# Kernel optimization log

Measured on AMD Instinct MI355X. Metric: run time of the kernel, lower is better.

## Reference

```python
import jax, jax.numpy as jnp
import numpy as np

B, N, K = 2, 8192, 16
C_IN, C_OUT, HID = 64, 256, 256
L, HEADS, DKQV = 2, 8, 32
D = HEADS * DKQV  # 256


def setup_inputs() -> dict:
    key = jax.random.key(0)
    ks = jax.random.split(key, 20)
    s = 0.02
    inp = {
        "xyzs": jax.random.normal(ks[0], (B, N, 3), jnp.float32),
        "features": jax.random.normal(ks[1], (B, N, C_IN), jnp.float32),
        "k_graph": jax.random.randint(ks[2], (B, N, K), 0, N),
        "W_in": jax.random.normal(ks[3], (C_IN, HID), jnp.float32) * s,
        "b_in": jnp.zeros((HID,), jnp.float32),
        "Wq": jax.random.normal(ks[4], (L, HID, D), jnp.float32) * s,
        "bq": jnp.zeros((L, D), jnp.float32),
        "Wk": jax.random.normal(ks[5], (L, HID, D), jnp.float32) * s,
        "bk": jnp.zeros((L, D), jnp.float32),
        "Wv": jax.random.normal(ks[6], (L, HID, D), jnp.float32) * s,
        "bv": jnp.zeros((L, D), jnp.float32),
        "Wp": jax.random.normal(ks[7], (L, 3, D), jnp.float32) * s,
        "bp": jnp.zeros((L, D), jnp.float32),
        "Wo": jax.random.normal(ks[8], (L, D, HID), jnp.float32) * s,
        "bo": jnp.zeros((L, HID), jnp.float32),
        "W_out": jax.random.normal(ks[9], (HID, C_OUT), jnp.float32) * s,
        "b_out": jnp.zeros((C_OUT,), jnp.float32),
    }
    return inp


def _gather(f, idx):
    # f: [B,N,D], idx: [B,N,K] -> [B,N,K,D]
    return jnp.take_along_axis(f[:, None], idx[..., None], axis=2)


def _knn_attn(xyz, f, idx, Wq, bq, Wk, bk, Wv, bv, Wp, bp, Wo, bo):
    b, n, _ = f.shape
    q = f @ Wq + bq                      # [B,N,D]
    k = f @ Wk + bk
    v = f @ Wv + bv
    k_nb = _gather(k, idx)               # [B,N,K,D]
    v_nb = _gather(v, idx)
    rel = xyz[:, :, None, :] - _gather(xyz, idx)   # [B,N,K,3]
    pos = rel @ Wp + bp                  # [B,N,K,D] relative positional encoding
    kh = (k_nb + pos).reshape(b, n, K, HEADS, DKQV)
    vh = (v_nb + pos).reshape(b, n, K, HEADS, DKQV)
    qh = q.reshape(b, n, HEADS, DKQV)
    logits = jnp.einsum('bnhd,bnkhd->bnhk', qh, kh) / np.sqrt(DKQV)
    attn = jax.nn.softmax(logits, axis=-1)          # softmax over K neighbors
    o = jnp.einsum('bnhk,bnkhd->bnhd', attn, vh).reshape(b, n, D)
    return o @ Wo + bo


def reference(xyzs, features, k_graph, W_in, b_in, Wq, bq, Wk, bk, Wv, bv,
              Wp, bp, Wo, bo, W_out, b_out):
    f = features @ W_in + b_in
    for l in range(L):
        res = f  # res_connection=True
        f = _knn_attn(xyzs, f, k_graph, Wq[l], bq[l], Wk[l], bk[l],
                      Wv[l], bv[l], Wp[l], bp[l], Wo[l], bo[l]) + res
    out = f @ W_out + b_out
    return jax.nn.leaky_relu(out, negative_slope=0.01)
```

## Files before the change

### kernel.cpp

```cpp
#include <hip/hip_runtime.h>
#include <hip/hip_bf16.h>

typedef __attribute__((ext_vector_type(8))) short bf16x8;
typedef __attribute__((ext_vector_type(4))) float f32x4;
typedef __attribute__((ext_vector_type(2))) _Float16 h2;
typedef __attribute__((ext_vector_type(8))) _Float16 h8;
typedef unsigned int uint;

constexpr int NPTS = 8192;
constexpr int BPTS = 16384;
constexpr int KNN  = 16;

__device__ __forceinline__ void gload16(const void* g, void* l) {
    __builtin_amdgcn_global_load_lds(
        (const __attribute__((address_space(1))) unsigned int*)g,
        (__attribute__((address_space(3))) unsigned int*)l, 16, 0, 0);
}

__device__ __forceinline__ uint packbf2(float a, float b) {
    union { __hip_bfloat16 h; unsigned short u; } ua, ub;
    ua.h = __float2bfloat16(a); ub.h = __float2bfloat16(b);
    return (uint)ua.u | ((uint)ub.u << 16);
}

template<int KD, bool RES, int OUTT, bool LRELU>
__global__ __launch_bounds__(256) void gemm_mfma(
    const __hip_bfloat16* __restrict__ A,
    const __hip_bfloat16* __restrict__ Bt,
    const float* __restrict__ b0, const float* __restrict__ b1,
    const float* __restrict__ b2,
    const __hip_bfloat16* __restrict__ res,
    void* __restrict__ Cout, int M, int N)
{
    __shared__ __align__(16) __hip_bfloat16 As[128 * 64];
    __shared__ __align__(16) __hip_bfloat16 Bs[128 * 64];

    const int tid  = threadIdx.x;
    const int lane = tid & 63;
    const int wid  = tid >> 6;
    const int wm   = (wid >> 1) * 64;
    const int wn   = (wid & 1) * 64;
    const int bm   = blockIdx.y * 128;
    const int bn   = blockIdx.x * 128;

    const int srow8 = lane >> 3;
    const int sslot = (lane & 7) ^ srow8;
    const int r = lane & 15;
    const int g = lane >> 4;

    f32x4 acc[4][4] = {};

    for (int k0 = 0; k0 < KD; k0 += 64) {
        #pragma unroll
        for (int p = 0; p < 4; ++p) {
            const int rowA = p * 32 + wid * 8 + srow8;
            gload16(&A[(size_t)(bm + rowA) * KD + k0 + sslot * 8],
                    (char*)As + (p * 32 + wid * 8) * 128);
            gload16(&Bt[(size_t)(bn + rowA) * KD + k0 + sslot * 8],
                    (char*)Bs + (p * 32 + wid * 8) * 128);
        }
        __syncthreads();

        bf16x8 af[2][4], bfr[2][4];
        #pragma unroll
        for (int s = 0; s < 2; ++s) {
            const int physA = (s * 4 + g) ^ (r & 7);
            #pragma unroll
            for (int mi = 0; mi < 4; ++mi)
                af[s][mi] = *(const bf16x8*)((const char*)As + (wm + mi * 16 + r) * 128 + physA * 16);
            #pragma unroll
            for (int ni = 0; ni < 4; ++ni)
                bfr[s][ni] = *(const bf16x8*)((const char*)Bs + (wn + ni * 16 + r) * 128 + physA * 16);
        }
        #pragma unroll
        for (int s = 0; s < 2; ++s)
            #pragma unroll
            for (int mi = 0; mi < 4; ++mi)
                #pragma unroll
                for (int ni = 0; ni < 4; ++ni)
                    acc[mi][ni] = __builtin_amdgcn_mfma_f32_16x16x32_bf16(
                        af[s][mi], bfr[s][ni], acc[mi][ni], 0, 0, 0);
        __syncthreads();
    }

    #pragma unroll
    for (int ni = 0; ni < 4; ++ni) {
        const int col = bn + wn + ni * 16 + r;
        const float* bsel = (col < 256) ? b0 : (col < 512 ? b1 : b2);
        const float bias = bsel[col & 255];
        #pragma unroll
        for (int mi = 0; mi < 4; ++mi) {
            #pragma unroll
            for (int q = 0; q < 4; ++q) {
                const int row = bm + wm + mi * 16 + g * 4 + q;
                float v = acc[mi][ni][q] + bias;
                if (RES)  v += __bfloat162float(res[(size_t)row * N + col]);
                if (LRELU) v = v > 0.f ? v : 0.01f * v;
                if (OUTT == 0)      ((float*)Cout)[(size_t)row * N + col] = v;
                else if (OUTT == 1) ((__hip_bfloat16*)Cout)[(size_t)row * N + col] = __float2bfloat16(v);
                else                ((_Float16*)Cout)[(size_t)row * N + col] = (_Float16)v;
            }
        }
    }
}

__global__ __launch_bounds__(256) void prep_kernel(
    const float* __restrict__ W_in, const float* __restrict__ Wq,
    const float* __restrict__ Wk,  const float* __restrict__ Wv,
    const float* __restrict__ Wo,  const float* __restrict__ W_out,
    const float* __restrict__ features,
    const float* __restrict__ Wp,  const float* __restrict__ bp,
    __hip_bfloat16* __restrict__ WtIn,  __hip_bfloat16* __restrict__ WtQKV,
    __hip_bfloat16* __restrict__ WtO,   __hip_bfloat16* __restrict__ WtOut,
    __hip_bfloat16* __restrict__ featb, _Float16* __restrict__ Wpb)
{
    const int b = blockIdx.x;
    if (b < 592) {
        const float* srcs[10] = {W_in, Wq, Wk, Wv, Wq + 65536, Wk + 65536,
                                 Wv + 65536, Wo, Wo + 65536, W_out};
        __hip_bfloat16* dsts[10] = {
            WtIn, WtQKV, WtQKV + 65536, WtQKV + 131072,
            WtQKV + 196608, WtQKV + 262144, WtQKV + 327680,
            WtO, WtO + 65536, WtOut};
        const int Ks[10]    = {64,256,256,256,256,256,256,256,256,256};
        const int start[10] = {0,16,80,144,208,272,336,400,464,528};
        int j = 0;
        #pragma unroll
        for (int i = 1; i < 10; ++i) if (b >= start[i]) j = i;
        const int t  = b - start[j];
        const int Kd = Ks[j];
        const int ntk = Kd >> 5;
        const int tn = t / ntk;
        const int tk = t - tn * ntk;

        __shared__ float s[32][33];
        const int tx = threadIdx.x & 31, ty = threadIdx.x >> 5;
        const float* src = srcs[j];
        #pragma unroll
        for (int i = 0; i < 4; ++i)
            s[ty + i * 8][tx] = src[(size_t)(tk * 32 + ty + i * 8) * 256 + tn * 32 + tx];
        __syncthreads();
        __hip_bfloat16* dst = dsts[j];
        #pragma unroll
        for (int i = 0; i < 4; ++i)
            dst[(size_t)(tn * 32 + ty + i * 8) * Kd + tk * 32 + tx] =
                __float2bfloat16(s[tx][ty + i * 8]);
    } else if (b < 1616) {
        const int i = (b - 592) * 1024 + threadIdx.x * 4;
        const float4 v = *(const float4*)&features[i];
        __hip_bfloat16 tmp[4] = {__float2bfloat16(v.x), __float2bfloat16(v.y),
                                 __float2bfloat16(v.z), __float2bfloat16(v.w)};
        *(uint2*)&featb[i] = *(const uint2*)tmp;
    } else {
        const int e8 = threadIdx.x * 8;
        const int l  = e8 >> 10;
        const int rr = (e8 >> 8) & 3;
        const int c  = e8 & 255;
        const float* src = (rr < 3) ? (Wp + (size_t)l * 768 + rr * 256 + c)
                                    : (bp + (size_t)l * 256 + c);
        const float4 f0 = ((const float4*)src)[0];
        const float4 f1 = ((const float4*)src)[1];
        _Float16 t[8] = {(_Float16)f0.x, (_Float16)f0.y, (_Float16)f0.z, (_Float16)f0.w,
                         (_Float16)f1.x, (_Float16)f1.y, (_Float16)f1.z, (_Float16)f1.w};
        *(uint4*)&Wpb[(size_t)l * 1024 + rr * 256 + c] = *(const uint4*)t;
    }
}

__global__ __launch_bounds__(256) void knn_attn_kernel(
    const float* __restrict__ xyz,
    const int*   __restrict__ idx,
    const _Float16* __restrict__ qkv,
    const _Float16* __restrict__ Wpb,
    __hip_bfloat16* __restrict__ o)
{
    const int tid = threadIdx.x;
    const int pt  = tid >> 7;
    const int lt  = tid & 127;
    const int p0  = blockIdx.x * 2;
    const int p   = p0 + pt;
    const int h   = lt >> 4;
    const int k   = lt & 15;

    __shared__ float s_rel[2][KNN][3];
    __shared__ float s_wq[2][8][4];
    __shared__ float s_attn[2][8][KNN];
    __shared__ float s_arel[2][8][3];
    __shared__ __align__(16) _Float16 v_lds[2][KNN][256];

    const int jrow = ((p >> 13) << 13) + idx[p * KNN + k];
    const h8* qp = (const h8*)(qkv + (size_t)p * 768 + h * 32);
    const h8* kp = (const h8*)(qkv + (size_t)jrow * 768 + 256 + h * 32);
    const h8 q0 = qp[0], q1 = qp[1];
    const h8 k0 = kp[0], k1 = kp[1];

    {
        const int w = tid >> 6, ln = tid & 63;
        #pragma unroll
        for (int c = 0; c < 4; ++c) {
            const int grE = w * 8 + c * 2;
            const int gr  = grE + (ln >> 5);
            const int ptw = grE >> 4, kkE = grE & 15;
            const int pg  = p0 + (gr >> 4);
            const int jr  = ((pg >> 13) << 13) + idx[pg * KNN + (gr & 15)];
            gload16(qkv + (size_t)jr * 768 + 512 + (ln & 31) * 8,
                    (char*)&v_lds[ptw][kkE][0]);
        }
    }

    if (tid < 32) {
        const int pp = tid >> 4, kk = tid & 15;
        const int pg = p0 + pp;
        const int jr = ((pg >> 13) << 13) + idx[pg * KNN + kk];
        s_rel[pp][kk][0] = xyz[pg * 3 + 0] - xyz[jr * 3 + 0];
        s_rel[pp][kk][1] = xyz[pg * 3 + 1] - xyz[jr * 3 + 1];
        s_rel[pp][kk][2] = xyz[pg * 3 + 2] - xyz[jr * 3 + 2];
    } else if (tid < 96) {
        const int t2 = tid - 32;
        const int pp = t2 >> 5, hh = (t2 >> 2) & 7, j = t2 & 3;
        const h8* qr = (const h8*)(qkv + (size_t)(p0 + pp) * 768 + hh * 32);
        const h8* wr = (const h8*)(Wpb + j * 256 + hh * 32);
        const h8 a0 = qr[0], a1 = qr[1], b0 = wr[0], b1 = wr[1];
        float acc = 0.f;
        #pragma unroll
        for (int i = 0; i < 4; ++i)
            acc = __builtin_amdgcn_fdot2(((const h2*)&a0)[i], ((const h2*)&b0)[i], acc, false);
        #pragma unroll
        for (int i = 0; i < 4; ++i)
            acc = __builtin_amdgcn_fdot2(((const h2*)&a1)[i], ((const h2*)&b1)[i], acc, false);
        s_wq[pp][hh][j] = acc;
    }

    float dot = 0.f;
    #pragma unroll
    for (int i = 0; i < 4; ++i)
        dot = __builtin_amdgcn_fdot2(((const h2*)&q0)[i], ((const h2*)&k0)[i], dot, false);
    #pragma unroll
    for (int i = 0; i < 4; ++i)
        dot = __builtin_amdgcn_fdot2(((const h2*)&q1)[i], ((const h2*)&k1)[i], dot, false);
    __syncthreads();

    const float r0 = s_rel[pt][k][0], r1 = s_rel[pt][k][1], r2 = s_rel[pt][k][2];
    const float logit = (dot + r0 * s_wq[pt][h][0] + r1 * s_wq[pt][h][1]
                             + r2 * s_wq[pt][h][2] + s_wq[pt][h][3])
                        * 0.1767766952966369f;
    float mx = logit;
    #pragma unroll
    for (int off = 8; off >= 1; off >>= 1)
        mx = fmaxf(mx, __shfl_xor(mx, off, 16));
    const float e = __expf(logit - mx);
    float den = e;
    #pragma unroll
    for (int off = 8; off >= 1; off >>= 1)
        den += __shfl_xor(den, off, 16);
    const float attn = e / den;
    s_attn[pt][h][k] = attn;

    float a0 = attn * r0, a1 = attn * r1, a2 = attn * r2;
    #pragma unroll
    for (int off = 8; off >= 1; off >>= 1) {
        a0 += __shfl_xor(a0, off, 16);
        a1 += __shfl_xor(a1, off, 16);
        a2 += __shfl_xor(a2, off, 16);
    }
    if (k == 0) {
        s_arel[pt][h][0] = a0;
        s_arel[pt][h][1] = a1;
        s_arel[pt][h][2] = a2;
    }
    __syncthreads();

    {
        const int ch = lt * 2;
        float ax = 0.f, ay = 0.f;
        #pragma unroll
        for (int kk = 0; kk < KNN; ++kk) {
            const float a = s_attn[pt][h][kk];
            const h2 vf = *(const h2*)&v_lds[pt][kk][ch];
            ax += a * (float)vf.x;
            ay += a * (float)vf.y;
        }
        const h2 w0 = *(const h2*)&Wpb[ch];
        const h2 w1 = *(const h2*)&Wpb[256 + ch];
        const h2 w2 = *(const h2*)&Wpb[512 + ch];
        const h2 w3 = *(const h2*)&Wpb[768 + ch];
        const float g0 = s_arel[pt][h][0], g1 = s_arel[pt][h][1], g2 = s_arel[pt][h][2];
        ax += g0 * (float)w0.x + g1 * (float)w1.x + g2 * (float)w2.x + (float)w3.x;
        ay += g0 * (float)w0.y + g1 * (float)w1.y + g2 * (float)w2.y + (float)w3.y;
        *(uint*)&o[(size_t)p * 256 + ch] = packbf2(ax, ay);
    }
}

extern "C" void kernel_launch(void* const* d_in, const int* in_sizes, int n_in,
                              void* d_out, int out_size, void* d_ws, size_t ws_size,
                              hipStream_t stream)
{
    const float* xyzs     = (const float*)d_in[0];
    const float* features = (const float*)d_in[1];
    const int*   k_graph  = (const int*)  d_in[2];
    const float* W_in     = (const float*)d_in[3];
    const float* b_in     = (const float*)d_in[4];
    const float* Wq       = (const float*)d_in[5];
    const float* bq       = (const float*)d_in[6];
    const float* Wk       = (const float*)d_in[7];
    const float* bk       = (const float*)d_in[8];
    const float* Wv       = (const float*)d_in[9];
    const float* bv       = (const float*)d_in[10];
    const float* Wp       = (const float*)d_in[11];
    const float* bp       = (const float*)d_in[12];
    const float* Wo       = (const float*)d_in[13];
    const float* bo       = (const float*)d_in[14];
    const float* W_out    = (const float*)d_in[15];
    const float* b_out    = (const float*)d_in[16];

    __hip_bfloat16* featb = (__hip_bfloat16*)d_ws;
    __hip_bfloat16* f     = featb + 1048576;
    _Float16*       qkv   = (_Float16*)(f + 4194304);
    __hip_bfloat16* ob    = (__hip_bfloat16*)(qkv + 12582912);
    __hip_bfloat16* WtIn  = ob + 4194304;
    __hip_bfloat16* WtQKV = WtIn + 16384;
    __hip_bfloat16* WtO   = WtQKV + 393216;
    __hip_bfloat16* WtOut = WtO + 131072;
    _Float16*       Wpb   = (_Float16*)(WtOut + 65536);

    prep_kernel<<<1617, 256, 0, stream>>>(W_in, Wq, Wk, Wv, Wo, W_out, features,
                                          Wp, bp, WtIn, WtQKV, WtO, WtOut,
                                          featb, Wpb);

    gemm_mfma<64, false, 1, false><<<dim3(2, 128), 256, 0, stream>>>(
        featb, WtIn, b_in, b_in, b_in, nullptr, f, BPTS, 256);

    for (int l = 0; l < 2; ++l) {
        gemm_mfma<256, false, 2, false><<<dim3(6, 128), 256, 0, stream>>>(
            f, WtQKV + (size_t)l * 196608,
            bq + l * 256, bk + l * 256, bv + l * 256, nullptr, qkv, BPTS, 768);

        knn_attn_kernel<<<dim3(BPTS / 2), 256, 0, stream>>>(
            xyzs, k_graph, qkv, Wpb + (size_t)l * 1024, ob);

        gemm_mfma<256, true, 1, false><<<dim3(2, 128), 256, 0, stream>>>(
            ob, WtO + (size_t)l * 65536,
            bo + l * 256, bo + l * 256, bo + l * 256, f, f, BPTS, 256);
    }

    gemm_mfma<256, false, 0, true><<<dim3(2, 128), 256, 0, stream>>>(
        f, WtOut, b_out, b_out, b_out, nullptr, (float*)d_out, BPTS, 256);
}
```

Measured before the change: 131.6 us.

## Fold W_in into layer-0 QKV weights, narrow GEMM tiles, widen attention blocks

Precomputes the product of W_in with the layer-0 Wq/Wk/Wv weights (and the matching biases) in a new small kernel, so layer-0 QKV comes from a K=64 GEMM over the raw features instead of a K=256 GEMM over f. The GEMM tile is narrowed from 128x128 to 128x64, doubling the grid to put more blocks on the GPU. The kNN attention kernel now handles 4 points per 512-thread block instead of 2 per 256. The fused weights are rounded to bf16 after the product, which adds a small amount of rounding error, and the narrower tile reuses each A tile across fewer output columns.

New measurement: 160.7 us. +22.1%, slower.

```diff
diff --git a/kernel.cpp b/kernel.cpp
--- a/kernel.cpp
+++ b/kernel.cpp
@@ -33,22 +33,22 @@
     void* __restrict__ Cout, int M, int N)
 {
     __shared__ __align__(16) __hip_bfloat16 As[128 * 64];
-    __shared__ __align__(16) __hip_bfloat16 Bs[128 * 64];
+    __shared__ __align__(16) __hip_bfloat16 Bs[64 * 64];
 
     const int tid  = threadIdx.x;
     const int lane = tid & 63;
     const int wid  = tid >> 6;
     const int wm   = (wid >> 1) * 64;
-    const int wn   = (wid & 1) * 64;
+    const int wn   = (wid & 1) * 32;
     const int bm   = blockIdx.y * 128;
-    const int bn   = blockIdx.x * 128;
+    const int bn   = blockIdx.x * 64;
 
     const int srow8 = lane >> 3;
     const int sslot = (lane & 7) ^ srow8;
     const int r = lane & 15;
     const int g = lane >> 4;
 
-    f32x4 acc[4][4] = {};
+    f32x4 acc[4][2] = {};
 
     for (int k0 = 0; k0 < KD; k0 += 64) {
         #pragma unroll
@@ -56,12 +56,16 @@
             const int rowA = p * 32 + wid * 8 + srow8;
             gload16(&A[(size_t)(bm + rowA) * KD + k0 + sslot * 8],
                     (char*)As + (p * 32 + wid * 8) * 128);
-            gload16(&Bt[(size_t)(bn + rowA) * KD + k0 + sslot * 8],
+        }
+        #pragma unroll
+        for (int p = 0; p < 2; ++p) {
+            const int rowB = p * 32 + wid * 8 + srow8;
+            gload16(&Bt[(size_t)(bn + rowB) * KD + k0 + sslot * 8],
                     (char*)Bs + (p * 32 + wid * 8) * 128);
         }
         __syncthreads();
 
-        bf16x8 af[2][4], bfr[2][4];
+        bf16x8 af[2][4], bfr[2][2];
         #pragma unroll
         for (int s = 0; s < 2; ++s) {
             const int physA = (s * 4 + g) ^ (r & 7);
@@ -69,7 +73,7 @@
             for (int mi = 0; mi < 4; ++mi)
                 af[s][mi] = *(const bf16x8*)((const char*)As + (wm + mi * 16 + r) * 128 + physA * 16);
             #pragma unroll
-            for (int ni = 0; ni < 4; ++ni)
+            for (int ni = 0; ni < 2; ++ni)
                 bfr[s][ni] = *(const bf16x8*)((const char*)Bs + (wn + ni * 16 + r) * 128 + physA * 16);
         }
         #pragma unroll
@@ -77,14 +81,14 @@
             #pragma unroll
             for (int mi = 0; mi < 4; ++mi)
                 #pragma unroll
-                for (int ni = 0; ni < 4; ++ni)
+                for (int ni = 0; ni < 2; ++ni)
                     acc[mi][ni] = __builtin_amdgcn_mfma_f32_16x16x32_bf16(
                         af[s][mi], bfr[s][ni], acc[mi][ni], 0, 0, 0);
         __syncthreads();
     }
 
     #pragma unroll
-    for (int ni = 0; ni < 4; ++ni) {
+    for (int ni = 0; ni < 2; ++ni) {
         const int col = bn + wn + ni * 16 + r;
         const float* bsel = (col < 256) ? b0 : (col < 512 ? b1 : b2);
         const float bias = bsel[col & 255];
@@ -166,7 +170,45 @@
     }
 }
 
-__global__ __launch_bounds__(256) void knn_attn_kernel(
+__global__ __launch_bounds__(256) void fuse_w1_kernel(
+    const float* __restrict__ W_in, const float* __restrict__ b_in,
+    const float* __restrict__ Wq, const float* __restrict__ bq,
+    const float* __restrict__ Wk, const float* __restrict__ bk,
+    const float* __restrict__ Wv, const float* __restrict__ bv,
+    __hip_bfloat16* __restrict__ WcT, float* __restrict__ bc)
+{
+    __shared__ float ws[256][32];
+    const int c0  = blockIdx.x * 32;
+    const int seg = c0 >> 8;
+    const int cs  = c0 & 255;
+    const float* Wsrc = seg == 0 ? Wq : (seg == 1 ? Wk : Wv);
+    const float* bsrc = seg == 0 ? bq : (seg == 1 ? bk : bv);
+    const int tx = threadIdx.x & 31, ty = threadIdx.x >> 5;
+
+    #pragma unroll 4
+    for (int i = 0; i < 32; ++i) {
+        const int k = i * 8 + ty;
+        ws[k][tx] = Wsrc[(size_t)k * 256 + cs + tx];
+    }
+    __syncthreads();
+
+    #pragma unroll
+    for (int rr = 0; rr < 8; ++rr) {
+        const int r = rr * 8 + ty;
+        float acc = 0.f;
+        for (int k = 0; k < 256; ++k)
+            acc += W_in[(size_t)r * 256 + k] * ws[k][tx];
+        WcT[(size_t)(c0 + tx) * 64 + r] = __float2bfloat16(acc);
+    }
+    if (ty == 0) {
+        float acc = 0.f;
+        for (int k = 0; k < 256; ++k)
+            acc += b_in[k] * ws[k][tx];
+        bc[c0 + tx] = acc + bsrc[cs + tx];
+    }
+}
+
+__global__ __launch_bounds__(512) void knn_attn_kernel(
     const float* __restrict__ xyz,
     const int*   __restrict__ idx,
     const _Float16* __restrict__ qkv,
@@ -176,16 +218,16 @@
     const int tid = threadIdx.x;
     const int pt  = tid >> 7;
     const int lt  = tid & 127;
-    const int p0  = blockIdx.x * 2;
+    const int p0  = blockIdx.x * 4;
     const int p   = p0 + pt;
     const int h   = lt >> 4;
     const int k   = lt & 15;
 
-    __shared__ float s_rel[2][KNN][3];
-    __shared__ float s_wq[2][8][4];
-    __shared__ float s_attn[2][8][KNN];
-    __shared__ float s_arel[2][8][3];
-    __shared__ __align__(16) _Float16 v_lds[2][KNN][256];
+    __shared__ float s_rel[4][KNN][3];
+    __shared__ float s_wq[4][8][4];
+    __shared__ float s_attn[4][8][KNN];
+    __shared__ float s_arel[4][8][3];
+    __shared__ __align__(16) _Float16 v_lds[4][KNN][256];
 
     const int jrow = ((p >> 13) << 13) + idx[p * KNN + k];
     const h8* qp = (const h8*)(qkv + (size_t)p * 768 + h * 32);
@@ -207,15 +249,15 @@
         }
     }
 
-    if (tid < 32) {
+    if (tid < 64) {
         const int pp = tid >> 4, kk = tid & 15;
         const int pg = p0 + pp;
         const int jr = ((pg >> 13) << 13) + idx[pg * KNN + kk];
         s_rel[pp][kk][0] = xyz[pg * 3 + 0] - xyz[jr * 3 + 0];
         s_rel[pp][kk][1] = xyz[pg * 3 + 1] - xyz[jr * 3 + 1];
         s_rel[pp][kk][2] = xyz[pg * 3 + 2] - xyz[jr * 3 + 2];
-    } else if (tid < 96) {
-        const int t2 = tid - 32;
+    } else if (tid < 192) {
+        const int t2 = tid - 64;
         const int pp = t2 >> 5, hh = (t2 >> 2) & 7, j = t2 & 3;
         const h8* qr = (const h8*)(qkv + (size_t)(p0 + pp) * 768 + hh * 32);
         const h8* wr = (const h8*)(Wpb + j * 256 + hh * 32);
@@ -321,27 +363,36 @@
     __hip_bfloat16* WtO   = WtQKV + 393216;
     __hip_bfloat16* WtOut = WtO + 131072;
     _Float16*       Wpb   = (_Float16*)(WtOut + 65536);
+    __hip_bfloat16* WcT   = (__hip_bfloat16*)(Wpb + 2048);
+    float*          bc    = (float*)(WcT + 49152);
 
     prep_kernel<<<1617, 256, 0, stream>>>(W_in, Wq, Wk, Wv, Wo, W_out, features,
                                           Wp, bp, WtIn, WtQKV, WtO, WtOut,
                                           featb, Wpb);
-
-    gemm_mfma<64, false, 1, false><<<dim3(2, 128), 256, 0, stream>>>(
+    fuse_w1_kernel<<<24, 256, 0, stream>>>(W_in, b_in, Wq, bq, Wk, bk, Wv, bv,
+                                           WcT, bc);
+
+    gemm_mfma<64, false, 1, false><<<dim3(4, 128), 256, 0, stream>>>(
         featb, WtIn, b_in, b_in, b_in, nullptr, f, BPTS, 256);
 
+    gemm_mfma<64, false, 2, false><<<dim3(12, 128), 256, 0, stream>>>(
+        featb, WcT, bc, bc + 256, bc + 512, nullptr, qkv, BPTS, 768);
+
     for (int l = 0; l < 2; ++l) {
-        gemm_mfma<256, false, 2, false><<<dim3(6, 128), 256, 0, stream>>>(
-            f, WtQKV + (size_t)l * 196608,
-            bq + l * 256, bk + l * 256, bv + l * 256, nullptr, qkv, BPTS, 768);
-
-        knn_attn_kernel<<<dim3(BPTS / 2), 256, 0, stream>>>(
+        if (l == 1) {
+            gemm_mfma<256, false, 2, false><<<dim3(12, 128), 256, 0, stream>>>(
+                f, WtQKV + 196608,
+                bq + 256, bk + 256, bv + 256, nullptr, qkv, BPTS, 768);
+        }
+
+        knn_attn_kernel<<<dim3(BPTS / 4), 512, 0, stream>>>(
             xyzs, k_graph, qkv, Wpb + (size_t)l * 1024, ob);
 
-        gemm_mfma<256, true, 1, false><<<dim3(2, 128), 256, 0, stream>>>(
+        gemm_mfma<256, true, 1, false><<<dim3(4, 128), 256, 0, stream>>>(
             ob, WtO + (size_t)l * 65536,
             bo + l * 256, bo + l * 256, bo + l * 256, f, f, BPTS, 256);
     }
 
-    gemm_mfma<256, false, 0, true><<<dim3(2, 128), 256, 0, stream>>>(
+    gemm_mfma<256, false, 0, true><<<dim3(4, 128), 256, 0, stream>>>(
         f, WtOut, b_out, b_out, b_out, nullptr, (float*)d_out, BPTS, 256);
 }
```

## Fold input projection into layer-0 QKV weights to shrink GEMM K dimension

Applied to the files above, without the earlier changes.

Precomputes combined weights W_in·Wqkv and a folded bias for layer 0 so the first QKV projection runs directly on the 64-channel input features instead of the 256-wide hidden state. This removes most of the arithmetic of the layer-0 QKV GEMM. In exchange it adds a small weight-folding GEMM, a bias-folding kernel and an extra prep segment, with slightly different bf16 rounding of the composed weights.

Result: slower. 139.4 us (+6.0%).

```diff
diff --git a/kernel.cpp b/kernel.cpp
--- a/kernel.cpp
+++ b/kernel.cpp
@@ -23,7 +23,7 @@
     return (uint)ua.u | ((uint)ub.u << 16);
 }
 
-template<int KD, bool RES, int OUTT, bool LRELU>
+template<int KD, bool RES, int OUTT, bool LRELU, int BN = 128, bool BIAS = true>
 __global__ __launch_bounds__(256) void gemm_mfma(
     const __hip_bfloat16* __restrict__ A,
     const __hip_bfloat16* __restrict__ Bt,
@@ -32,23 +32,26 @@
     const __hip_bfloat16* __restrict__ res,
     void* __restrict__ Cout, int M, int N)
 {
+    constexpr int WN = BN / 2;
+    constexpr int NB = WN / 16;
+
     __shared__ __align__(16) __hip_bfloat16 As[128 * 64];
-    __shared__ __align__(16) __hip_bfloat16 Bs[128 * 64];
+    __shared__ __align__(16) __hip_bfloat16 Bs[BN * 64];
 
     const int tid  = threadIdx.x;
     const int lane = tid & 63;
     const int wid  = tid >> 6;
     const int wm   = (wid >> 1) * 64;
-    const int wn   = (wid & 1) * 64;
+    const int wn   = (wid & 1) * WN;
     const int bm   = blockIdx.y * 128;
-    const int bn   = blockIdx.x * 128;
+    const int bn   = blockIdx.x * BN;
 
     const int srow8 = lane >> 3;
     const int sslot = (lane & 7) ^ srow8;
     const int r = lane & 15;
     const int g = lane >> 4;
 
-    f32x4 acc[4][4] = {};
+    f32x4 acc[4][NB] = {};
 
     for (int k0 = 0; k0 < KD; k0 += 64) {
         #pragma unroll
@@ -56,12 +59,16 @@
             const int rowA = p * 32 + wid * 8 + srow8;
             gload16(&A[(size_t)(bm + rowA) * KD + k0 + sslot * 8],
                     (char*)As + (p * 32 + wid * 8) * 128);
-            gload16(&Bt[(size_t)(bn + rowA) * KD + k0 + sslot * 8],
+        }
+        #pragma unroll
+        for (int p = 0; p < BN / 32; ++p) {
+            const int rowB = p * 32 + wid * 8 + srow8;
+            gload16(&Bt[(size_t)(bn + rowB) * KD + k0 + sslot * 8],
                     (char*)Bs + (p * 32 + wid * 8) * 128);
         }
         __syncthreads();
 
-        bf16x8 af[2][4], bfr[2][4];
+        bf16x8 af[2][4], bfr[2][NB];
         #pragma unroll
         for (int s = 0; s < 2; ++s) {
             const int physA = (s * 4 + g) ^ (r & 7);
@@ -69,7 +76,7 @@
             for (int mi = 0; mi < 4; ++mi)
                 af[s][mi] = *(const bf16x8*)((const char*)As + (wm + mi * 16 + r) * 128 + physA * 16);
             #pragma unroll
-            for (int ni = 0; ni < 4; ++ni)
+            for (int ni = 0; ni < NB; ++ni)
                 bfr[s][ni] = *(const bf16x8*)((const char*)Bs + (wn + ni * 16 + r) * 128 + physA * 16);
         }
         #pragma unroll
@@ -77,17 +84,20 @@
             #pragma unroll
             for (int mi = 0; mi < 4; ++mi)
                 #pragma unroll
-                for (int ni = 0; ni < 4; ++ni)
+                for (int ni = 0; ni < NB; ++ni)
                     acc[mi][ni] = __builtin_amdgcn_mfma_f32_16x16x32_bf16(
                         af[s][mi], bfr[s][ni], acc[mi][ni], 0, 0, 0);
         __syncthreads();
     }
 
     #pragma unroll
-    for (int ni = 0; ni < 4; ++ni) {
+    for (int ni = 0; ni < NB; ++ni) {
         const int col = bn + wn + ni * 16 + r;
-        const float* bsel = (col < 256) ? b0 : (col < 512 ? b1 : b2);
-        const float bias = bsel[col & 255];
+        float bias = 0.f;
+        if (BIAS) {
+            const float* bsel = (col < 256) ? b0 : (col < 512 ? b1 : b2);
+            bias = bsel[col & 255];
+        }
         #pragma unroll
         for (int mi = 0; mi < 4; ++mi) {
             #pragma unroll
@@ -112,7 +122,8 @@
     const float* __restrict__ Wp,  const float* __restrict__ bp,
     __hip_bfloat16* __restrict__ WtIn,  __hip_bfloat16* __restrict__ WtQKV,
     __hip_bfloat16* __restrict__ WtO,   __hip_bfloat16* __restrict__ WtOut,
-    __hip_bfloat16* __restrict__ featb, _Float16* __restrict__ Wpb)
+    __hip_bfloat16* __restrict__ featb, _Float16* __restrict__ Wpb,
+    __hip_bfloat16* __restrict__ WinB)
 {
     const int b = blockIdx.x;
     if (b < 592) {
@@ -151,7 +162,7 @@
         __hip_bfloat16 tmp[4] = {__float2bfloat16(v.x), __float2bfloat16(v.y),
                                  __float2bfloat16(v.z), __float2bfloat16(v.w)};
         *(uint2*)&featb[i] = *(const uint2*)tmp;
-    } else {
+    } else if (b == 1616) {
         const int e8 = threadIdx.x * 8;
         const int l  = e8 >> 10;
         const int rr = (e8 >> 8) & 3;
@@ -163,7 +174,30 @@
         _Float16 t[8] = {(_Float16)f0.x, (_Float16)f0.y, (_Float16)f0.z, (_Float16)f0.w,
                          (_Float16)f1.x, (_Float16)f1.y, (_Float16)f1.z, (_Float16)f1.w};
         *(uint4*)&Wpb[(size_t)l * 1024 + rr * 256 + c] = *(const uint4*)t;
-    }
+    } else {
+        const int i = (b - 1617) * 1024 + threadIdx.x * 4;
+        const float4 v = *(const float4*)&W_in[i];
+        __hip_bfloat16 tmp[4] = {__float2bfloat16(v.x), __float2bfloat16(v.y),
+                                 __float2bfloat16(v.z), __float2bfloat16(v.w)};
+        *(uint2*)&WinB[i] = *(const uint2*)tmp;
+    }
+}
+
+__global__ __launch_bounds__(256) void qkv1_bias_kernel(
+    const float* __restrict__ b_in,
+    const float* __restrict__ Wq, const float* __restrict__ bq,
+    const float* __restrict__ Wk, const float* __restrict__ bk,
+    const float* __restrict__ Wv, const float* __restrict__ bv,
+    float* __restrict__ bc)
+{
+    const int seg = blockIdx.x;
+    const int c   = threadIdx.x;
+    const float* W  = seg == 0 ? Wq : (seg == 1 ? Wk : Wv);
+    const float* bb = seg == 0 ? bq : (seg == 1 ? bk : bv);
+    float acc = 0.f;
+    for (int k = 0; k < 256; ++k)
+        acc += b_in[k] * W[(size_t)k * 256 + c];
+    bc[seg * 256 + c] = acc + bb[c];
 }
 
 __global__ __launch_bounds__(256) void knn_attn_kernel(
@@ -321,18 +355,30 @@
     __hip_bfloat16* WtO   = WtQKV + 393216;
     __hip_bfloat16* WtOut = WtO + 131072;
     _Float16*       Wpb   = (_Float16*)(WtOut + 65536);
-
-    prep_kernel<<<1617, 256, 0, stream>>>(W_in, Wq, Wk, Wv, Wo, W_out, features,
+    __hip_bfloat16* WcT   = (__hip_bfloat16*)(Wpb + 2048);
+    float*          bc    = (float*)(WcT + 49152);
+    __hip_bfloat16* WinB  = (__hip_bfloat16*)(bc + 768);
+
+    prep_kernel<<<1633, 256, 0, stream>>>(W_in, Wq, Wk, Wv, Wo, W_out, features,
                                           Wp, bp, WtIn, WtQKV, WtO, WtOut,
-                                          featb, Wpb);
+                                          featb, Wpb, WinB);
+    qkv1_bias_kernel<<<3, 256, 0, stream>>>(b_in, Wq, bq, Wk, bk, Wv, bv, bc);
+
+    gemm_mfma<256, false, 1, false, 64, false><<<dim3(1, 6), 256, 0, stream>>>(
+        WtQKV, WinB, nullptr, nullptr, nullptr, nullptr, WcT, 768, 64);
 
     gemm_mfma<64, false, 1, false><<<dim3(2, 128), 256, 0, stream>>>(
         featb, WtIn, b_in, b_in, b_in, nullptr, f, BPTS, 256);
 
+    gemm_mfma<64, false, 2, false><<<dim3(6, 128), 256, 0, stream>>>(
+        featb, WcT, bc, bc + 256, bc + 512, nullptr, qkv, BPTS, 768);
+
     for (int l = 0; l < 2; ++l) {
-        gemm_mfma<256, false, 2, false><<<dim3(6, 128), 256, 0, stream>>>(
-            f, WtQKV + (size_t)l * 196608,
-            bq + l * 256, bk + l * 256, bv + l * 256, nullptr, qkv, BPTS, 768);
+        if (l == 1) {
+            gemm_mfma<256, false, 2, false><<<dim3(6, 128), 256, 0, stream>>>(
+                f, WtQKV + 196608,
+                bq + 256, bk + 256, bv + 256, nullptr, qkv, BPTS, 768);
+        }
 
         knn_attn_kernel<<<dim3(BPTS / 2), 256, 0, stream>>>(
             xyzs, k_graph, qkv, Wpb + (size_t)l * 1024, ob);
```

## Stage V in transposed-friendly LDS layout and use ds_read_b64_tr_b16 with fdot2 for PV

Applied to the files above, without the earlier changes.

Replaces the global-to-LDS async copy of neighbor V rows with register loads, followed by a swizzled LDS store into a layout suited to the transpose read instruction. The P·V accumulation now reads transposed fp16 pairs via ds_read_b64_tr_b16 and uses fdot2 against fp16 attention weights, so each thread computes two channels instead of a serial 16-step scalar FMA loop. The intent is to cut LDS read count and ALU work in the weighted sum. In exchange it quantizes the attention weights to fp16, writes scalar bf16 outputs instead of packed pairs, and loses the overlap that the async LDS load gave with the QK computation.

After: 133.3 us. No clear change (+1.3%).

```diff
diff --git a/kernel.cpp b/kernel.cpp
--- a/kernel.cpp
+++ b/kernel.cpp
@@ -15,12 +15,6 @@
     __builtin_amdgcn_global_load_lds(
         (const __attribute__((address_space(1))) unsigned int*)g,
         (__attribute__((address_space(3))) unsigned int*)l, 16, 0, 0);
-}
-
-__device__ __forceinline__ uint packbf2(float a, float b) {
-    union { __hip_bfloat16 h; unsigned short u; } ua, ub;
-    ua.h = __float2bfloat16(a); ub.h = __float2bfloat16(b);
-    return (uint)ua.u | ((uint)ub.u << 16);
 }
 
 template<int KD, bool RES, int OUTT, bool LRELU>
@@ -178,34 +172,31 @@
     const int lt  = tid & 127;
     const int p0  = blockIdx.x * 2;
     const int p   = p0 + pt;
-    const int h   = lt >> 4;
+    const int hh  = lt >> 4;
     const int k   = lt & 15;
 
     __shared__ float s_rel[2][KNN][3];
     __shared__ float s_wq[2][8][4];
-    __shared__ float s_attn[2][8][KNN];
+    __shared__ _Float16 s_ah[2][8][KNN];
     __shared__ float s_arel[2][8][3];
-    __shared__ __align__(16) _Float16 v_lds[2][KNN][256];
+    __shared__ __align__(16) char v_raw[16384];
 
     const int jrow = ((p >> 13) << 13) + idx[p * KNN + k];
-    const h8* qp = (const h8*)(qkv + (size_t)p * 768 + h * 32);
-    const h8* kp = (const h8*)(qkv + (size_t)jrow * 768 + 256 + h * 32);
+    const h8* qp = (const h8*)(qkv + (size_t)p * 768 + hh * 32);
+    const h8* kp = (const h8*)(qkv + (size_t)jrow * 768 + 256 + hh * 32);
     const h8 q0 = qp[0], q1 = qp[1];
     const h8 k0 = kp[0], k1 = kp[1];
 
-    {
-        const int w = tid >> 6, ln = tid & 63;
-        #pragma unroll
-        for (int c = 0; c < 4; ++c) {
-            const int grE = w * 8 + c * 2;
-            const int gr  = grE + (ln >> 5);
-            const int ptw = grE >> 4, kkE = grE & 15;
-            const int pg  = p0 + (gr >> 4);
-            const int jr  = ((pg >> 13) << 13) + idx[pg * KNN + (gr & 15)];
-            gload16(qkv + (size_t)jr * 768 + 512 + (ln & 31) * 8,
-                    (char*)&v_lds[ptw][kkE][0]);
-        }
-    }
+    const int sk = lt >> 3;
+    const int c4 = lt & 7;
+    const int jr_st = ((p >> 13) << 13) + idx[p * KNN + sk];
+    const uint4* vsrc = (const uint4*)(qkv + (size_t)jr_st * 768 + 512 + c4 * 8);
+    const uint4 st0 = vsrc[0];
+    const uint4 st1 = vsrc[8];
+    const uint4 st2 = vsrc[16];
+    const uint4 st3 = vsrc[24];
+    const int dbase = pt * 8192 + (sk >> 2) * 2048 + (c4 >> 1) * 128
+                    + (sk & 3) * 32 + (c4 & 1) * 16;
 
     if (tid < 32) {
         const int pp = tid >> 4, kk = tid & 15;
@@ -216,9 +207,9 @@
         s_rel[pp][kk][2] = xyz[pg * 3 + 2] - xyz[jr * 3 + 2];
     } else if (tid < 96) {
         const int t2 = tid - 32;
-        const int pp = t2 >> 5, hh = (t2 >> 2) & 7, j = t2 & 3;
-        const h8* qr = (const h8*)(qkv + (size_t)(p0 + pp) * 768 + hh * 32);
-        const h8* wr = (const h8*)(Wpb + j * 256 + hh * 32);
+        const int pp = t2 >> 5, hq = (t2 >> 2) & 7, j = t2 & 3;
+        const h8* qr = (const h8*)(qkv + (size_t)(p0 + pp) * 768 + hq * 32);
+        const h8* wr = (const h8*)(Wpb + j * 256 + hq * 32);
         const h8 a0 = qr[0], a1 = qr[1], b0 = wr[0], b1 = wr[1];
         float acc = 0.f;
         #pragma unroll
@@ -227,7 +218,7 @@
         #pragma unroll
         for (int i = 0; i < 4; ++i)
             acc = __builtin_amdgcn_fdot2(((const h2*)&a1)[i], ((const h2*)&b1)[i], acc, false);
-        s_wq[pp][hh][j] = acc;
+        s_wq[pp][hq][j] = acc;
     }
 
     float dot = 0.f;
@@ -240,8 +231,8 @@
     __syncthreads();
 
     const float r0 = s_rel[pt][k][0], r1 = s_rel[pt][k][1], r2 = s_rel[pt][k][2];
-    const float logit = (dot + r0 * s_wq[pt][h][0] + r1 * s_wq[pt][h][1]
-                             + r2 * s_wq[pt][h][2] + s_wq[pt][h][3])
+    const float logit = (dot + r0 * s_wq[pt][hh][0] + r1 * s_wq[pt][hh][1]
+                             + r2 * s_wq[pt][hh][2] + s_wq[pt][hh][3])
                         * 0.1767766952966369f;
     float mx = logit;
     #pragma unroll
@@ -253,7 +244,7 @@
     for (int off = 8; off >= 1; off >>= 1)
         den += __shfl_xor(den, off, 16);
     const float attn = e / den;
-    s_attn[pt][h][k] = attn;
+    s_ah[pt][hh][k] = (_Float16)attn;
 
     float a0 = attn * r0, a1 = attn * r1, a2 = attn * r2;
     #pragma unroll
@@ -263,30 +254,63 @@
         a2 += __shfl_xor(a2, off, 16);
     }
     if (k == 0) {
-        s_arel[pt][h][0] = a0;
-        s_arel[pt][h][1] = a1;
-        s_arel[pt][h][2] = a2;
-    }
+        s_arel[pt][hh][0] = a0;
+        s_arel[pt][hh][1] = a1;
+        s_arel[pt][hh][2] = a2;
+    }
+
+    *(uint4*)(v_raw + dbase +    0) = st0;
+    *(uint4*)(v_raw + dbase +  512) = st1;
+    *(uint4*)(v_raw + dbase + 1024) = st2;
+    *(uint4*)(v_raw + dbase + 1536) = st3;
     __syncthreads();
 
     {
-        const int ch = lt * 2;
-        float ax = 0.f, ay = 0.f;
-        #pragma unroll
-        for (int kk = 0; kk < KNN; ++kk) {
-            const float a = s_attn[pt][h][kk];
-            const h2 vf = *(const h2*)&v_lds[pt][kk][ch];
-            ax += a * (float)vf.x;
-            ay += a * (float)vf.y;
-        }
-        const h2 w0 = *(const h2*)&Wpb[ch];
-        const h2 w1 = *(const h2*)&Wpb[256 + ch];
-        const h2 w2 = *(const h2*)&Wpb[512 + ch];
-        const h2 w3 = *(const h2*)&Wpb[768 + ch];
-        const float g0 = s_arel[pt][h][0], g1 = s_arel[pt][h][1], g2 = s_arel[pt][h][2];
-        ax += g0 * (float)w0.x + g1 * (float)w1.x + g2 * (float)w2.x + (float)w3.x;
-        ay += g0 * (float)w0.y + g1 * (float)w1.y + g2 * (float)w2.y + (float)w3.y;
-        *(uint*)&o[(size_t)p * 256 + ch] = packbf2(ax, ay);
+        const int w   = tid >> 6;
+        const int l   = tid & 63;
+        const int pt2 = w >> 1;
+        const int H   = w & 1;
+        const int g   = l >> 4;
+        const int li  = l & 15;
+        const int chA = H * 128 + g * 16 + li;
+        const int chB = chA + 64;
+        const int hA  = chA >> 5, hB = chB >> 5;
+        const int p2  = p0 + pt2;
+
+        const unsigned vg = (unsigned)(size_t)
+            (__attribute__((address_space(3))) char*)(v_raw + pt2 * 8192 + H * 1024 + l * 8);
+
+        uint2 rA0, rA1, rA2, rA3, rB0, rB1, rB2, rB3;
+        asm volatile("ds_read_b64_tr_b16 %0, %1 offset:0"    : "=v"(rA0) : "v"(vg));
+        asm volatile("ds_read_b64_tr_b16 %0, %1 offset:2048" : "=v"(rA1) : "v"(vg));
+        asm volatile("ds_read_b64_tr_b16 %0, %1 offset:4096" : "=v"(rA2) : "v"(vg));
+        asm volatile("ds_read_b64_tr_b16 %0, %1 offset:6144" : "=v"(rA3) : "v"(vg));
+        asm volatile("ds_read_b64_tr_b16 %0, %1 offset:512"  : "=v"(rB0) : "v"(vg));
+        asm volatile("ds_read_b64_tr_b16 %0, %1 offset:2560" : "=v"(rB1) : "v"(vg));
+        asm volatile("ds_read_b64_tr_b16 %0, %1 offset:4608" : "=v"(rB2) : "v"(vg));
+        asm volatile("ds_read_b64_tr_b16 %0, %1 offset:6656" : "=v"(rB3) : "v"(vg));
+        asm volatile("s_waitcnt lgkmcnt(0)" ::: "memory");
+        __builtin_amdgcn_sched_barrier(0);
+
+        const h2* aA = (const h2*)&s_ah[pt2][hA][0];
+        const h2* aB = (const h2*)&s_ah[pt2][hB][0];
+
+        float oA = 0.f, oB = 0.f;
+        #define PVKT(rr, aa, acc, kt)                                             \
+            acc = __builtin_amdgcn_fdot2(aa[2*kt],   *(const h2*)&rr.x, acc, false); \
+            acc = __builtin_amdgcn_fdot2(aa[2*kt+1], *(const h2*)&rr.y, acc, false);
+        PVKT(rA0, aA, oA, 0) PVKT(rA1, aA, oA, 1) PVKT(rA2, aA, oA, 2) PVKT(rA3, aA, oA, 3)
+        PVKT(rB0, aB, oB, 0) PVKT(rB1, aB, oB, 1) PVKT(rB2, aB, oB, 2) PVKT(rB3, aB, oB, 3)
+        #undef PVKT
+
+        const float gA0 = s_arel[pt2][hA][0], gA1 = s_arel[pt2][hA][1], gA2 = s_arel[pt2][hA][2];
+        const float gB0 = s_arel[pt2][hB][0], gB1 = s_arel[pt2][hB][1], gB2 = s_arel[pt2][hB][2];
+        oA += gA0 * (float)Wpb[chA] + gA1 * (float)Wpb[256 + chA]
+            + gA2 * (float)Wpb[512 + chA] + (float)Wpb[768 + chA];
+        oB += gB0 * (float)Wpb[chB] + gB1 * (float)Wpb[256 + chB]
+            + gB2 * (float)Wpb[512 + chB] + (float)Wpb[768 + chB];
+        o[(size_t)p2 * 256 + chA] = __float2bfloat16(oA);
+        o[(size_t)p2 * 256 + chB] = __float2bfloat16(oB);
     }
 }
 
```
